# Performance work log

Measured on AMD Instinct MI355X. Metric: run time of the kernel, lower is better.

Reference implementation:

```python
import jax, jax.numpy as jnp
import numpy as np

B, S, D = 2, 2048, 2048
H = 16
Q_LORA, KV_LORA = 1536, 512
D_NOPE, D_ROPE = 128, 64
D_QK = D_NOPE + D_ROPE  # 192
D_V = 128
EPS = 1e-6
SCALE = D_QK ** -0.5


def rms_norm(x, w):
    var = jnp.mean(jnp.square(x), axis=-1, keepdims=True)
    return x * jax.lax.rsqrt(var + EPS) * w


def apply_rotary_emb(x, freqs_cis):
    # x: [B, S, h, dr]; freqs_cis: [S, dr//2, 2] (cos, sin); interleaved pairs
    b, s, h, dr = x.shape
    xp = x.reshape(b, s, h, dr // 2, 2)
    x0, x1 = xp[..., 0], xp[..., 1]
    cos = freqs_cis[None, :, None, :, 0]
    sin = freqs_cis[None, :, None, :, 1]
    o0 = x0 * cos - x1 * sin
    o1 = x0 * sin + x1 * cos
    return jnp.stack([o0, o1], axis=-1).reshape(b, s, h, dr)


def setup_inputs() -> dict:
    key = jax.random.key(0)
    ks = jax.random.split(key, 8)
    std = 0.02
    x = jax.random.normal(ks[0], (B, S, D), jnp.float32)
    inv_freq = 1.0 / (10000.0 ** (np.arange(0, D_ROPE, 2, dtype=np.float32) / D_ROPE))
    ang = np.outer(np.arange(S, dtype=np.float32), inv_freq)  # [S, 32]
    freqs_cis = jnp.asarray(np.stack([np.cos(ang), np.sin(ang)], axis=-1))
    return {
        'x': x,
        'freqs_cis': freqs_cis,
        'Wqa': jax.random.normal(ks[1], (Q_LORA, D), jnp.float32) * std,
        'q_a_ln_w': jnp.ones((Q_LORA,), jnp.float32),
        'Wqb': jax.random.normal(ks[2], (H * D_QK, Q_LORA), jnp.float32) * std,
        'Wkva': jax.random.normal(ks[3], (KV_LORA + D_ROPE, D), jnp.float32) * std,
        'kv_a_ln_w': jnp.ones((KV_LORA,), jnp.float32),
        'Wkvb': jax.random.normal(ks[4], (H * (D_NOPE + D_V), KV_LORA), jnp.float32) * std,
        'Wo': jax.random.normal(ks[5], (D, H * D_V), jnp.float32) * std,
    }


def reference(x, freqs_cis, Wqa, q_a_ln_w, Wqb, Wkva, kv_a_ln_w, Wkvb, Wo):
    # Low-rank Q projection: down -> RMSNorm -> up
    q = rms_norm(jnp.einsum('bsd,rd->bsr', x, Wqa), q_a_ln_w)
    q = jnp.einsum('bsr,er->bse', q, Wqb).reshape(B, S, H, D_QK)
    q_nope, q_pe = q[..., :D_NOPE], q[..., D_NOPE:]
    q = jnp.concatenate([q_nope, apply_rotary_emb(q_pe, freqs_cis)], axis=-1)

    # Low-rank KV projection with shared (MQA) rope part
    kv = jnp.einsum('bsd,ed->bse', x, Wkva)
    kv_c, k_pe = kv[..., :KV_LORA], kv[..., KV_LORA:]
    kv_c = rms_norm(kv_c, kv_a_ln_w)
    k_pe = apply_rotary_emb(k_pe[:, :, None, :], freqs_cis)  # [B,S,1,D_ROPE]
    kv = jnp.einsum('bsr,er->bse', kv_c, Wkvb).reshape(B, S, H, D_NOPE + D_V)
    k_nope, v = kv[..., :D_NOPE], kv[..., D_NOPE:]
    k = jnp.concatenate(
        [k_nope, jnp.broadcast_to(k_pe, (B, S, H, D_ROPE))], axis=-1)

    # Causal SDPA with scale = qk_head_dim ** -0.5
    scores = jnp.einsum('bqhd,bkhd->bhqk', q, k) * SCALE
    causal = jnp.tril(jnp.ones((S, S), bool))
    scores = jnp.where(causal[None, None], scores, jnp.finfo(scores.dtype).min)
    probs = jax.nn.softmax(scores, axis=-1)
    out = jnp.einsum('bhqk,bkhd->bqhd', probs, v).reshape(B, S, H * D_V)
    return jnp.einsum('bse,de->bsd', out, Wo)
```

## Files before the change

kernel.cpp:

```cpp
#include <hip/hip_runtime.h>
#include <math.h>

#define B_ 2
#define S_ 2048
#define D_ 2048
#define H_ 16
#define QLORA 1536
#define KVLORA 512
#define DN 128
#define DR 64
#define DQK 192
#define DV 128
#define EPSF 1e-6f
#define SCALEF 0.07216878364870322f

typedef short short8 __attribute__((ext_vector_type(8)));
typedef float float4v __attribute__((ext_vector_type(4)));

__device__ __forceinline__ unsigned short f2bf(float f) {
    union { float f; unsigned u; } x; x.f = f;
    unsigned r = x.u + 0x7fffu + ((x.u >> 16) & 1u);
    return (unsigned short)(r >> 16);
}
__device__ __forceinline__ float bf2f(unsigned short u) {
    union { unsigned u; float f; } x; x.u = (unsigned)u << 16;
    return x.f;
}

#define GLD16(src, dst)                                                        \
    __builtin_amdgcn_global_load_lds(                                          \
        (const __attribute__((address_space(1))) void*)(src),                  \
        (__attribute__((address_space(3))) void*)(dst), 16, 0, 0)

__global__ __launch_bounds__(256) void conv_all(
        const float* __restrict__ s0, unsigned short* __restrict__ d0, long e0,
        const float* __restrict__ s1, unsigned short* __restrict__ d1, long e1,
        const float* __restrict__ s2, unsigned short* __restrict__ d2, long e2,
        const float* __restrict__ s3, unsigned short* __restrict__ d3, long e3,
        const float* __restrict__ s4, unsigned short* __restrict__ d4, long e4,
        const float* __restrict__ s5, unsigned short* __restrict__ d5) {
    long c = (long)blockIdx.x * 256 + threadIdx.x;
    const float* src;
    unsigned short* dst;
    if      (c < e0) { src = s0; dst = d0; }
    else if (c < e1) { src = s1; dst = d1; c -= e0; }
    else if (c < e2) { src = s2; dst = d2; c -= e1; }
    else if (c < e3) { src = s3; dst = d3; c -= e2; }
    else if (c < e4) { src = s4; dst = d4; c -= e3; }
    else             { src = s5; dst = d5; c -= e4; }
    const float* p = src + c * 8;
    float4 a = *(const float4*)(p);
    float4 b = *(const float4*)(p + 4);
    union { short8 v; unsigned short u[8]; } t;
    t.u[0] = f2bf(a.x); t.u[1] = f2bf(a.y); t.u[2] = f2bf(a.z); t.u[3] = f2bf(a.w);
    t.u[4] = f2bf(b.x); t.u[5] = f2bf(b.y); t.u[6] = f2bf(b.z); t.u[7] = f2bf(b.w);
    *(short8*)&dst[c * 8] = t.v;
}

#define GBM 128
#define GBN 128
#define GBK 64

template <typename OT>
__global__ __launch_bounds__(256) void gemm_t(const unsigned short* __restrict__ A,
                                              const unsigned short* __restrict__ W,
                                              OT* __restrict__ C,
                                              int M, int N, int K) {
    __shared__ unsigned short As[GBM * GBK];
    __shared__ unsigned short Ws[GBN * GBK];

    const int tid = threadIdx.x;
    const int w = tid >> 6, lane = tid & 63;
    const int l16 = lane & 15, quad = lane >> 4;
    const int wm = (w >> 1) * 64, wn = (w & 1) * 64;
    const int row0 = blockIdx.y * GBM, col0 = blockIdx.x * GBN;

    const int rL  = lane >> 3;
    const int c8g = (lane & 7) ^ rL;
    const int swzk[2] = { (((0 * 4) + quad) ^ (l16 & 7)) * 8,
                          (((1 * 4) + quad) ^ (l16 & 7)) * 8 };

    const float4v zf = {0.f, 0.f, 0.f, 0.f};
    float4v acc[4][4] = {{zf, zf, zf, zf}, {zf, zf, zf, zf},
                         {zf, zf, zf, zf}, {zf, zf, zf, zf}};

    for (int k0 = 0; k0 < K; k0 += GBK) {
        __syncthreads();
#pragma unroll
        for (int j = 0; j < 4; ++j) {
            const int ch = w * 4 + j;
            const int r = ch * 8 + rL;
            GLD16(&A[(size_t)(row0 + r) * K + k0 + c8g * 8], &As[ch * 512]);
            GLD16(&W[(size_t)(col0 + r) * K + k0 + c8g * 8], &Ws[ch * 512]);
        }
        __syncthreads();

#pragma unroll
        for (int kk = 0; kk < 2; ++kk) {
            const int swz = swzk[kk];
            short8 af[4], bf[4];
#pragma unroll
            for (int mi = 0; mi < 4; ++mi)
                af[mi] = *(const short8*)&As[(wm + mi * 16 + l16) * GBK + swz];
#pragma unroll
            for (int ni = 0; ni < 4; ++ni)
                bf[ni] = *(const short8*)&Ws[(wn + ni * 16 + l16) * GBK + swz];
#pragma unroll
            for (int mi = 0; mi < 4; ++mi)
#pragma unroll
                for (int ni = 0; ni < 4; ++ni)
                    acc[mi][ni] = __builtin_amdgcn_mfma_f32_16x16x32_bf16(af[mi], bf[ni], acc[mi][ni], 0, 0, 0);
        }
    }

#pragma unroll
    for (int mi = 0; mi < 4; ++mi)
#pragma unroll
        for (int ni = 0; ni < 4; ++ni)
#pragma unroll
            for (int r = 0; r < 4; ++r) {
                size_t idx = (size_t)(row0 + wm + mi * 16 + quad * 4 + r) * N + col0 + wn + ni * 16 + l16;
                if constexpr (sizeof(OT) == 2) C[idx] = f2bf(acc[mi][ni][r]);
                else                           C[idx] = acc[mi][ni][r];
            }
}

__global__ __launch_bounds__(256) void gemm_kv(const unsigned short* __restrict__ A,
                                               const unsigned short* __restrict__ W,
                                               unsigned short* __restrict__ kvbb,
                                               unsigned short* __restrict__ Kbf,
                                               int M, int N, int K) {
    __shared__ unsigned short As[GBM * GBK];
    __shared__ unsigned short Ws[GBN * GBK];

    const int tid = threadIdx.x;
    const int w = tid >> 6, lane = tid & 63;
    const int l16 = lane & 15, quad = lane >> 4;
    const int wm = (w >> 1) * 64, wn = (w & 1) * 64;
    const int row0 = blockIdx.y * GBM, col0 = blockIdx.x * GBN;
    const int h = blockIdx.x >> 1, vhalf = blockIdx.x & 1;

    const int rL  = lane >> 3;
    const int c8g = (lane & 7) ^ rL;
    const int swzk[2] = { (((0 * 4) + quad) ^ (l16 & 7)) * 8,
                          (((1 * 4) + quad) ^ (l16 & 7)) * 8 };

    const float4v zf = {0.f, 0.f, 0.f, 0.f};
    float4v acc[4][4] = {{zf, zf, zf, zf}, {zf, zf, zf, zf},
                         {zf, zf, zf, zf}, {zf, zf, zf, zf}};

    for (int k0 = 0; k0 < K; k0 += GBK) {
        __syncthreads();
#pragma unroll
        for (int j = 0; j < 4; ++j) {
            const int ch = w * 4 + j;
            const int r = ch * 8 + rL;
            GLD16(&A[(size_t)(row0 + r) * K + k0 + c8g * 8], &As[ch * 512]);
            GLD16(&W[(size_t)(col0 + r) * K + k0 + c8g * 8], &Ws[ch * 512]);
        }
        __syncthreads();

#pragma unroll
        for (int kk = 0; kk < 2; ++kk) {
            const int swz = swzk[kk];
            short8 af[4], bf[4];
#pragma unroll
            for (int mi = 0; mi < 4; ++mi)
                af[mi] = *(const short8*)&As[(wm + mi * 16 + l16) * GBK + swz];
#pragma unroll
            for (int ni = 0; ni < 4; ++ni)
                bf[ni] = *(const short8*)&Ws[(wn + ni * 16 + l16) * GBK + swz];
#pragma unroll
            for (int mi = 0; mi < 4; ++mi)
#pragma unroll
                for (int ni = 0; ni < 4; ++ni)
                    acc[mi][ni] = __builtin_amdgcn_mfma_f32_16x16x32_bf16(af[mi], bf[ni], acc[mi][ni], 0, 0, 0);
        }
    }

#pragma unroll
    for (int mi = 0; mi < 4; ++mi)
#pragma unroll
        for (int ni = 0; ni < 4; ++ni)
#pragma unroll
            for (int r = 0; r < 4; ++r) {
                const int row = row0 + wm + mi * 16 + quad * 4 + r;
                const int d = wn + ni * 16 + l16;
                const unsigned short v = f2bf(acc[mi][ni][r]);
                if (vhalf) {
                    kvbb[(size_t)row * N + col0 + d] = v;
                } else {
                    const int b = row >> 11, s = row & (S_ - 1);
                    Kbf[((size_t)(b * H_ + h) * S_ + s) * DQK + d] = v;
                }
            }
}

__global__ __launch_bounds__(256) void rmsnorm_b(const float* __restrict__ X,
                                                 const float* __restrict__ w,
                                                 unsigned short* __restrict__ Y,
                                                 int n, int ld) {
    __shared__ float tmp[4];
    const int row = blockIdx.x;
    const int tid = threadIdx.x;
    const float* x = X + (size_t)row * ld;

    float ss = 0.f;
    for (int c = tid; c < n; c += 256) {
        float v = x[c];
        ss = fmaf(v, v, ss);
    }
#pragma unroll
    for (int off = 32; off; off >>= 1) ss += __shfl_xor(ss, off, 64);
    if ((tid & 63) == 0) tmp[tid >> 6] = ss;
    __syncthreads();
    ss = tmp[0] + tmp[1] + tmp[2] + tmp[3];
    float r = rsqrtf(ss / (float)n + EPSF);

    for (int c = tid; c < n; c += 256)
        Y[(size_t)row * n + c] = f2bf(x[c] * r * w[c]);
}

__global__ __launch_bounds__(256) void kv_post(const float* __restrict__ KV,
                                               const float* __restrict__ w,
                                               const float* __restrict__ fc,
                                               unsigned short* __restrict__ kvcb,
                                               unsigned short* __restrict__ Kbf,
                                               int ldkv) {
    __shared__ float tmp[4];
    const int row = blockIdx.x;
    const int s = row & (S_ - 1);
    const int b = row >> 11;
    const int tid = threadIdx.x;
    const float* kv = KV + (size_t)row * ldkv;

    float ss = 0.f;
#pragma unroll
    for (int c = tid; c < KVLORA; c += 256) {
        float v = kv[c];
        ss = fmaf(v, v, ss);
    }
#pragma unroll
    for (int off = 32; off; off >>= 1) ss += __shfl_xor(ss, off, 64);
    if ((tid & 63) == 0) tmp[tid >> 6] = ss;
    __syncthreads();
    ss = tmp[0] + tmp[1] + tmp[2] + tmp[3];
    float r = rsqrtf(ss / (float)KVLORA + EPSF);

#pragma unroll
    for (int c = tid; c < KVLORA; c += 256)
        kvcb[(size_t)row * KVLORA + c] = f2bf(kv[c] * r * w[c]);

    if (tid < 32) {
        int i = tid;
        float c0 = fc[(s * 32 + i) * 2 + 0];
        float s0 = fc[(s * 32 + i) * 2 + 1];
        float x0 = kv[KVLORA + 2 * i];
        float x1 = kv[KVLORA + 2 * i + 1];
        unsigned short b0 = f2bf(x0 * c0 - x1 * s0);
        unsigned short b1 = f2bf(x0 * s0 + x1 * c0);
#pragma unroll
        for (int h = 0; h < H_; ++h) {
            unsigned short* kp = Kbf + ((size_t)(b * H_ + h) * S_ + s) * DQK + DN;
            kp[2 * i]     = b0;
            kp[2 * i + 1] = b1;
        }
    }
}

__global__ __launch_bounds__(256) void pack_vt(const unsigned short* __restrict__ kvbb,
                                               unsigned short* __restrict__ Vt) {
    __shared__ unsigned short T[DV][72];
    const int st = blockIdx.x;
    const int bh = blockIdx.y;
    const int b = bh >> 4, h = bh & 15;
    const int s0 = st * 64;
    const int tid = threadIdx.x;

    for (int c = tid; c < 64 * 16; c += 256) {
        int sp = c >> 4, ch = c & 15;
        short8 v = *(const short8*)&kvbb[(size_t)(b * S_ + s0 + sp) * (H_ * 256) + h * 256 + DN + ch * 8];
        union { short8 v; unsigned short u[8]; } t; t.v = v;
        int dv = ch * 8;
#pragma unroll
        for (int e = 0; e < 8; ++e) T[dv + e][sp] = t.u[e];
    }
    __syncthreads();
    for (int c = tid; c < 128 * 8; c += 256) {
        int dv = c >> 3, ch = c & 7;
        *(short8*)&Vt[((size_t)bh * DV + dv) * S_ + s0 + ch * 8] = *(short8*)&T[dv][ch * 8];
    }
}

#define QTILES 16
#define PROW 76

__global__ __launch_bounds__(512, 1) void flash_mfma(const unsigned short* __restrict__ Qb,
                                                     const float* __restrict__ fc,
                                                     const unsigned short* __restrict__ Kbf,
                                                     const unsigned short* __restrict__ Vt,
                                                     unsigned short* __restrict__ Ob) {
    __shared__ unsigned short Ks[2][64 * 192];
    __shared__ unsigned short Vs[2][128 * 64];
    __shared__ unsigned short Ps[8][16][PROW];

    const int bh = blockIdx.x;
    const int bx = blockIdx.y;
    const int b = bh >> 4, h = bh & 15;
    const int tid = threadIdx.x;
    const int w = tid >> 6, lane = tid & 63;
    const int l16 = lane & 15, quad = lane >> 4;
    const int sw = l16 & 7;

    const unsigned short* Kg = Kbf + (size_t)bh * S_ * DQK;
    const unsigned short* Vg = Vt + (size_t)bh * DV * S_;

    auto stage = [&](int kt_, int bufi) {
        const int kb_ = kt_ * 64;
#pragma unroll
        for (int i_ = 0; i_ < 3; ++i_) {
            int ch = (w * 3 + i_) * 64 + lane;
            int r_ = ch / 24, c_ = ch - r_ * 24;
            GLD16(&Kg[(size_t)(kb_ + r_) * DQK + ((c_ ^ (r_ & 7)) << 3)],
                  &Ks[bufi][(w * 3 + i_) * 512]);
        }
#pragma unroll
        for (int i_ = 0; i_ < 2; ++i_) {
            int ch = (w * 2 + i_) * 64 + lane;
            int r_ = ch >> 3, c_ = ch & 7;
            GLD16(&Vg[(size_t)r_ * S_ + kb_ + ((c_ ^ (r_ & 7)) << 3)],
                  &Vs[bufi][(w * 2 + i_) * 512]);
        }
    };

    for (int half = 0; half < 2; ++half) {
        const int qt = half ? (QTILES - 1 - bx) : bx;
        const int q0 = qt * 128;
        const int ntiles = 2 * qt + 2;
        const int wr0 = q0 + w * 16;

        stage(0, 0);

        short8 a_q[6];
        {
            const int s = wr0 + l16;
            const unsigned short* qrow = Qb + (size_t)(b * S_ + s) * (H_ * DQK) + h * DQK;
#pragma unroll
            for (int i = 0; i < 6; ++i) {
                short8 t = *(const short8*)&qrow[i * 32 + quad * 8];
                if (i >= 4) {
                    union { short8 v; unsigned short u[8]; } x; x.v = t;
#pragma unroll
                    for (int j = 0; j < 4; ++j) {
                        int ip = (i - 4) * 16 + quad * 4 + j;
                        float c0 = fc[(s * 32 + ip) * 2 + 0];
                        float s0 = fc[(s * 32 + ip) * 2 + 1];
                        float x0 = bf2f(x.u[2 * j]);
                        float x1 = bf2f(x.u[2 * j + 1]);
                        x.u[2 * j]     = f2bf(x0 * c0 - x1 * s0);
                        x.u[2 * j + 1] = f2bf(x0 * s0 + x1 * c0);
                    }
                    t = x.v;
                }
                a_q[i] = t;
            }
        }

        const float4v zf = {0.f, 0.f, 0.f, 0.f};
        float4v o_acc[8] = {zf, zf, zf, zf, zf, zf, zf, zf};
        float l_r[4] = {0.f, 0.f, 0.f, 0.f};

        int buf = 0;
        for (int kt = 0; kt < ntiles; ++kt) {
            const int kb = kt * 64;

            __builtin_amdgcn_s_barrier();
            if (kt + 1 < ntiles) {
                stage(kt + 1, buf ^ 1);
                asm volatile("s_waitcnt vmcnt(5)" ::: "memory");
            } else {
                asm volatile("s_waitcnt vmcnt(0)" ::: "memory");
            }
            __builtin_amdgcn_sched_barrier(0);
            __builtin_amdgcn_s_barrier();
            __builtin_amdgcn_sched_barrier(0);

            if (kb <= wr0 + 15) {
                const unsigned short* Kb_ = Ks[buf];
                const unsigned short* Vb_ = Vs[buf];

                float4v sc[4] = {zf, zf, zf, zf};
                __builtin_amdgcn_s_setprio(1);
#pragma unroll
                for (int i = 0; i < 6; ++i) {
                    short8 bk[4];
#pragma unroll
                    for (int kg = 0; kg < 4; ++kg)
                        bk[kg] = *(const short8*)&Kb_[(kg * 16 + l16) * 192 + (((i * 4 + quad) ^ sw) << 3)];
#pragma unroll
                    for (int kg = 0; kg < 4; ++kg)
                        sc[kg] = __builtin_amdgcn_mfma_f32_16x16x32_bf16(a_q[i], bk[kg], sc[kg], 0, 0, 0);
                }
                __builtin_amdgcn_s_setprio(0);

                const bool mneed = (kb + 63 > wr0);
#pragma unroll
                for (int kg = 0; kg < 4; ++kg) {
                    const int key = kb + kg * 16 + l16;
#pragma unroll
                    for (int r = 0; r < 4; ++r) {
                        float p = __expf(sc[kg][r] * SCALEF);
                        if (mneed && key > wr0 + quad * 4 + r) p = 0.f;
                        l_r[r] += p;
                        Ps[w][quad * 4 + r][kg * 16 + l16] = f2bf(p);
                    }
                }

                __builtin_amdgcn_s_setprio(1);
#pragma unroll
                for (int kc = 0; kc < 2; ++kc) {
                    short8 pa = *(const short8*)&Ps[w][l16][kc * 32 + quad * 8];
#pragma unroll
                    for (int dvt = 0; dvt < 8; ++dvt) {
                        short8 vb = *(const short8*)&Vb_[(dvt * 16 + l16) * 64 + (((kc * 4 + quad) ^ sw) << 3)];
                        o_acc[dvt] = __builtin_amdgcn_mfma_f32_16x16x32_bf16(pa, vb, o_acc[dvt], 0, 0, 0);
                    }
                }
                __builtin_amdgcn_s_setprio(0);
            }
            buf ^= 1;
        }

#pragma unroll
        for (int r = 0; r < 4; ++r) {
            float t = l_r[r];
            t += __shfl_xor(t, 1);
            t += __shfl_xor(t, 2);
            t += __shfl_xor(t, 4);
            t += __shfl_xor(t, 8);
            l_r[r] = t;
        }
#pragma unroll
        for (int r = 0; r < 4; ++r) {
            float inv = 1.f / l_r[r];
            int row = wr0 + quad * 4 + r;
            unsigned short* op = Ob + (size_t)(b * S_ + row) * (H_ * DV) + h * DV;
#pragma unroll
            for (int dvt = 0; dvt < 8; ++dvt)
                op[dvt * 16 + l16] = f2bf(o_acc[dvt][r] * inv);
        }
    }
}

extern "C" void kernel_launch(void* const* d_in, const int* in_sizes, int n_in,
                              void* d_out, int out_size, void* d_ws, size_t ws_size,
                              hipStream_t stream) {
    const float* x    = (const float*)d_in[0];
    const float* fc   = (const float*)d_in[1];
    const float* Wqa  = (const float*)d_in[2];
    const float* qlw  = (const float*)d_in[3];
    const float* Wqb  = (const float*)d_in[4];
    const float* Wkva = (const float*)d_in[5];
    const float* kvw  = (const float*)d_in[6];
    const float* Wkvb = (const float*)d_in[7];
    const float* Wo   = (const float*)d_in[8];
    float* out = (float*)d_out;

    const int M = B_ * S_;
    const int NQKV = QLORA + 640;
    char* wsb = (char*)d_ws;

    unsigned short* qb  = (unsigned short*)wsb;
    unsigned short* Wob = (unsigned short*)(wsb + 25165824);
    char* R2 = wsb + 50331648;
    float*          qlkv  = (float*)R2;
    unsigned short* xb    = (unsigned short*)(R2 + 35651584);
    unsigned short* Wcat  = (unsigned short*)(R2 + 52428800);
    unsigned short* kvbb  = (unsigned short*)R2;
    unsigned short* attnb = (unsigned short*)R2;
    char* R3 = R2 + 67108864;
    unsigned short* qlatb = (unsigned short*)R3;
    unsigned short* Wqbb  = (unsigned short*)(R3 + 12582912);
    unsigned short* Kbf   = (unsigned short*)R3;
    char* R4 = R3 + 25165824;
    unsigned short* kvcb  = (unsigned short*)(R4 + 1048576);
    unsigned short* Wkvbb = (unsigned short*)(R4 + 5242880);
    unsigned short* Vt    = (unsigned short*)R4;

    {
        const long e0 = 1048576;
        const long e1 = e0 + 393216;
        const long e2 = e1 + 147456;
        const long e3 = e2 + 589824;
        const long e4 = e3 + 262144;
        const long tot = e4 + 524288;
        conv_all<<<(int)(tot / 256), 256, 0, stream>>>(
            x, xb, e0,
            Wqa, Wcat, e1,
            Wkva, Wcat + (size_t)QLORA * D_, e2,
            Wqb, Wqbb, e3,
            Wkvb, Wkvbb, e4,
            Wo, Wob);
    }

    gemm_t<float><<<dim3(NQKV / GBN, M / GBM), 256, 0, stream>>>(xb, Wcat, qlkv, M, NQKV, D_);

    rmsnorm_b<<<M, 256, 0, stream>>>(qlkv, qlw, qlatb, QLORA, NQKV);

    gemm_t<unsigned short><<<dim3(H_ * DQK / GBN, M / GBM), 256, 0, stream>>>(qlatb, Wqbb, qb, M, H_ * DQK, QLORA);

    kv_post<<<M, 256, 0, stream>>>(qlkv + QLORA, kvw, fc, kvcb, Kbf, NQKV);

    gemm_kv<<<dim3(H_ * 256 / GBN, M / GBM), 256, 0, stream>>>(kvcb, Wkvbb, kvbb, Kbf, M, H_ * 256, KVLORA);

    pack_vt<<<dim3(S_ / 64, B_ * H_), 256, 0, stream>>>(kvbb, Vt);

    flash_mfma<<<dim3(B_ * H_, QTILES / 2), 512, 0, stream>>>(qb, fc, Kbf, Vt, attnb);

    gemm_t<float><<<dim3(D_ / GBN, M / GBM), 256, 0, stream>>>(attnb, Wob, out, M, D_, D_);
}
```

Before: 466.9 us.

## Replace projection GEMMs with double-buffered 256x256-tile eight-wave GEMM

```diff
diff --git a/kernel.cpp b/kernel.cpp
--- a/kernel.cpp
+++ b/kernel.cpp
@@ -125,73 +125,116 @@
             }
 }
 
-__global__ __launch_bounds__(256) void gemm_kv(const unsigned short* __restrict__ A,
-                                               const unsigned short* __restrict__ W,
-                                               unsigned short* __restrict__ kvbb,
-                                               unsigned short* __restrict__ Kbf,
-                                               int M, int N, int K) {
-    __shared__ unsigned short As[GBM * GBK];
-    __shared__ unsigned short Ws[GBN * GBK];
+#define TBM 256
+#define TBN 256
+#define TBK 64
+
+template <int MODE>
+__global__ __launch_bounds__(512, 2) void gemm8(const unsigned short* __restrict__ A,
+                                                const unsigned short* __restrict__ W,
+                                                void* __restrict__ Cp,
+                                                unsigned short* __restrict__ Cs,
+                                                int M, int N, int K) {
+    __shared__ unsigned short As[2][TBM * TBK];
+    __shared__ unsigned short Ws[2][TBN * TBK];
 
     const int tid = threadIdx.x;
     const int w = tid >> 6, lane = tid & 63;
     const int l16 = lane & 15, quad = lane >> 4;
-    const int wm = (w >> 1) * 64, wn = (w & 1) * 64;
-    const int row0 = blockIdx.y * GBM, col0 = blockIdx.x * GBN;
-    const int h = blockIdx.x >> 1, vhalf = blockIdx.x & 1;
-
-    const int rL  = lane >> 3;
-    const int c8g = (lane & 7) ^ rL;
-    const int swzk[2] = { (((0 * 4) + quad) ^ (l16 & 7)) * 8,
-                          (((1 * 4) + quad) ^ (l16 & 7)) * 8 };
+    const int wm = (w >> 2) * 128, wn = (w & 3) * 64;
+    const int row0 = blockIdx.y * TBM, col0 = blockIdx.x * TBN;
+    const int NT = K / TBK;
+
+    auto stage = [&](int t_, int bufi) {
+        const int k0 = t_ * TBK;
+#pragma unroll
+        for (int i_ = 0; i_ < 4; ++i_) {
+            const int ch = i_ * 512 + w * 64 + lane;
+            const int r_ = ch >> 3, c_ = ch & 7;
+            GLD16(&A[(size_t)(row0 + r_) * K + k0 + ((c_ ^ (r_ & 7)) << 3)],
+                  &As[bufi][(i_ * 512 + w * 64) * 8]);
+        }
+#pragma unroll
+        for (int i_ = 0; i_ < 4; ++i_) {
+            const int ch = i_ * 512 + w * 64 + lane;
+            const int r_ = ch >> 3, c_ = ch & 7;
+            GLD16(&W[(size_t)(col0 + r_) * K + k0 + ((c_ ^ (r_ & 7)) << 3)],
+                  &Ws[bufi][(i_ * 512 + w * 64) * 8]);
+        }
+    };
 
     const float4v zf = {0.f, 0.f, 0.f, 0.f};
-    float4v acc[4][4] = {{zf, zf, zf, zf}, {zf, zf, zf, zf},
-                         {zf, zf, zf, zf}, {zf, zf, zf, zf}};
-
-    for (int k0 = 0; k0 < K; k0 += GBK) {
-        __syncthreads();
-#pragma unroll
-        for (int j = 0; j < 4; ++j) {
-            const int ch = w * 4 + j;
-            const int r = ch * 8 + rL;
-            GLD16(&A[(size_t)(row0 + r) * K + k0 + c8g * 8], &As[ch * 512]);
-            GLD16(&W[(size_t)(col0 + r) * K + k0 + c8g * 8], &Ws[ch * 512]);
-        }
-        __syncthreads();
-
-#pragma unroll
-        for (int kk = 0; kk < 2; ++kk) {
-            const int swz = swzk[kk];
-            short8 af[4], bf[4];
-#pragma unroll
-            for (int mi = 0; mi < 4; ++mi)
-                af[mi] = *(const short8*)&As[(wm + mi * 16 + l16) * GBK + swz];
-#pragma unroll
-            for (int ni = 0; ni < 4; ++ni)
-                bf[ni] = *(const short8*)&Ws[(wn + ni * 16 + l16) * GBK + swz];
-#pragma unroll
-            for (int mi = 0; mi < 4; ++mi)
-#pragma unroll
-                for (int ni = 0; ni < 4; ++ni)
-                    acc[mi][ni] = __builtin_amdgcn_mfma_f32_16x16x32_bf16(af[mi], bf[ni], acc[mi][ni], 0, 0, 0);
-        }
-    }
-
-#pragma unroll
-    for (int mi = 0; mi < 4; ++mi)
+    float4v acc[8][4];
+#pragma unroll
+    for (int mi = 0; mi < 8; ++mi)
+#pragma unroll
+        for (int ni = 0; ni < 4; ++ni) acc[mi][ni] = zf;
+
+    stage(0, 0);
+    stage(1, 1);
+    asm volatile("s_waitcnt vmcnt(8)" ::: "memory");
+    __builtin_amdgcn_sched_barrier(0);
+    __builtin_amdgcn_s_barrier();
+    __builtin_amdgcn_sched_barrier(0);
+
+    for (int t = 0; t < NT; ++t) {
+        const int buf = t & 1;
+        const unsigned short* Ab = As[buf];
+        const unsigned short* Wb = Ws[buf];
+
+        short8 bfr[2][4];
+#pragma unroll
+        for (int kk = 0; kk < 2; ++kk)
+#pragma unroll
+            for (int ni = 0; ni < 4; ++ni) {
+                const int Rn = wn + ni * 16 + l16;
+                bfr[kk][ni] = *(const short8*)&Wb[Rn * TBK + (((kk * 4 + quad) ^ (l16 & 7)) << 3)];
+            }
+#pragma unroll
+        for (int mi = 0; mi < 8; ++mi) {
+            const int Rm = wm + mi * 16 + l16;
+            short8 a0 = *(const short8*)&Ab[Rm * TBK + (((0 + quad) ^ (l16 & 7)) << 3)];
+            short8 a1 = *(const short8*)&Ab[Rm * TBK + (((4 + quad) ^ (l16 & 7)) << 3)];
+#pragma unroll
+            for (int ni = 0; ni < 4; ++ni) {
+                acc[mi][ni] = __builtin_amdgcn_mfma_f32_16x16x32_bf16(a0, bfr[0][ni], acc[mi][ni], 0, 0, 0);
+                acc[mi][ni] = __builtin_amdgcn_mfma_f32_16x16x32_bf16(a1, bfr[1][ni], acc[mi][ni], 0, 0, 0);
+            }
+        }
+
+        __builtin_amdgcn_s_barrier();
+        if (t + 2 < NT) {
+            stage(t + 2, buf);
+            asm volatile("s_waitcnt vmcnt(8)" ::: "memory");
+        } else if (t + 1 < NT) {
+            asm volatile("s_waitcnt vmcnt(0)" ::: "memory");
+        }
+        __builtin_amdgcn_sched_barrier(0);
+        __builtin_amdgcn_s_barrier();
+        __builtin_amdgcn_sched_barrier(0);
+    }
+
+#pragma unroll
+    for (int mi = 0; mi < 8; ++mi)
 #pragma unroll
         for (int ni = 0; ni < 4; ++ni)
 #pragma unroll
             for (int r = 0; r < 4; ++r) {
                 const int row = row0 + wm + mi * 16 + quad * 4 + r;
-                const int d = wn + ni * 16 + l16;
-                const unsigned short v = f2bf(acc[mi][ni][r]);
-                if (vhalf) {
-                    kvbb[(size_t)row * N + col0 + d] = v;
+                const int col = col0 + wn + ni * 16 + l16;
+                if constexpr (MODE == 0) {
+                    ((float*)Cp)[(size_t)row * N + col] = acc[mi][ni][r];
+                } else if constexpr (MODE == 1) {
+                    ((unsigned short*)Cp)[(size_t)row * N + col] = f2bf(acc[mi][ni][r]);
                 } else {
-                    const int b = row >> 11, s = row & (S_ - 1);
-                    Kbf[((size_t)(b * H_ + h) * S_ + s) * DQK + d] = v;
+                    const int h = col >> 8, within = col & 255;
+                    const unsigned short v = f2bf(acc[mi][ni][r]);
+                    if (within < 128) {
+                        const int b = row >> 11, s = row & (S_ - 1);
+                        Cs[((size_t)(b * H_ + h) * S_ + s) * DQK + within] = v;
+                    } else {
+                        ((unsigned short*)Cp)[(size_t)row * N + col] = v;
+                    }
                 }
             }
 }
@@ -390,7 +433,6 @@
                 const unsigned short* Vb_ = Vs[buf];
 
                 float4v sc[4] = {zf, zf, zf, zf};
-                __builtin_amdgcn_s_setprio(1);
 #pragma unroll
                 for (int i = 0; i < 6; ++i) {
                     short8 bk[4];
@@ -401,7 +443,6 @@
                     for (int kg = 0; kg < 4; ++kg)
                         sc[kg] = __builtin_amdgcn_mfma_f32_16x16x32_bf16(a_q[i], bk[kg], sc[kg], 0, 0, 0);
                 }
-                __builtin_amdgcn_s_setprio(0);
 
                 const bool mneed = (kb + 63 > wr0);
 #pragma unroll
@@ -416,7 +457,6 @@
                     }
                 }
 
-                __builtin_amdgcn_s_setprio(1);
 #pragma unroll
                 for (int kc = 0; kc < 2; ++kc) {
                     short8 pa = *(const short8*)&Ps[w][l16][kc * 32 + quad * 8];
@@ -426,7 +466,6 @@
                         o_acc[dvt] = __builtin_amdgcn_mfma_f32_16x16x32_bf16(pa, vb, o_acc[dvt], 0, 0, 0);
                     }
                 }
-                __builtin_amdgcn_s_setprio(0);
             }
             buf ^= 1;
         }
@@ -507,15 +546,15 @@
 
     rmsnorm_b<<<M, 256, 0, stream>>>(qlkv, qlw, qlatb, QLORA, NQKV);
 
-    gemm_t<unsigned short><<<dim3(H_ * DQK / GBN, M / GBM), 256, 0, stream>>>(qlatb, Wqbb, qb, M, H_ * DQK, QLORA);
+    gemm8<1><<<dim3(H_ * DQK / TBN, M / TBM), 512, 0, stream>>>(qlatb, Wqbb, qb, nullptr, M, H_ * DQK, QLORA);
 
     kv_post<<<M, 256, 0, stream>>>(qlkv + QLORA, kvw, fc, kvcb, Kbf, NQKV);
 
-    gemm_kv<<<dim3(H_ * 256 / GBN, M / GBM), 256, 0, stream>>>(kvcb, Wkvbb, kvbb, Kbf, M, H_ * 256, KVLORA);
+    gemm8<2><<<dim3(H_ * 256 / TBN, M / TBM), 512, 0, stream>>>(kvcb, Wkvbb, kvbb, Kbf, M, H_ * 256, KVLORA);
 
     pack_vt<<<dim3(S_ / 64, B_ * H_), 256, 0, stream>>>(kvbb, Vt);
 
     flash_mfma<<<dim3(B_ * H_, QTILES / 2), 512, 0, stream>>>(qb, fc, Kbf, Vt, attnb);
 
-    gemm_t<float><<<dim3(D_ / GBN, M / GBM), 256, 0, stream>>>(attnb, Wob, out, M, D_, D_);
-}
+    gemm8<0><<<dim3(D_ / TBN, M / TBM), 512, 0, stream>>>(attnb, Wob, out, nullptr, M, D_, D_);
+}
```

Measured after the change: 447.4 us. -4.2%, faster.
